# Kernel optimization log

Hardware: AMD Instinct MI355X
Metric: run time of the kernel (lower is better)

The kernel has to match this reference:

```python
import jax, jax.numpy as jnp
import numpy as np

WORD = 512
ED = 64


def setup_inputs() -> dict:
    key = jax.random.key(0)
    ks = jax.random.split(key, 7)
    x = jax.random.normal(ks[0], (4, 4096, WORD), dtype=jnp.float32)
    # Dense layer params (kernel + bias) for query/key/value projections
    s = 1.0 / np.sqrt(WORD)
    Wq = jax.random.normal(ks[1], (WORD, ED), dtype=jnp.float32) * s
    Wk = jax.random.normal(ks[2], (WORD, ED), dtype=jnp.float32) * s
    Wv = jax.random.normal(ks[3], (WORD, ED), dtype=jnp.float32) * s
    bq = jnp.zeros((ED,), dtype=jnp.float32)
    bk = jnp.zeros((ED,), dtype=jnp.float32)
    bv = jnp.zeros((ED,), dtype=jnp.float32)
    return {"x": x, "Wq": Wq, "bq": bq, "Wk": Wk, "bk": bk, "Wv": Wv, "bv": bv}


def reference(x, Wq, bq, Wk, bk, Wv, bv):
    # Q, K, V: [B, S, ED]
    Q = jnp.einsum('bsw,we->bse', x, Wq) + bq
    K = jnp.einsum('bsw,we->bse', x, Wk) + bk
    V = jnp.einsum('bsw,we->bse', x, Wv) + bv
    scale = 1.0 / jnp.sqrt(jnp.float32(ED))
    score = jnp.einsum('bqe,bke->bqk', Q, K) * scale  # [B, S, S]
    attn = jax.nn.softmax(score, axis=-1)
    Z = jnp.einsum('bqk,bke->bqe', attn, V)  # [B, S, ED]
    return Z
```

## Files before the change

### kernel.cpp

```cpp
#include <hip/hip_runtime.h>
#include <cstdint>


typedef __bf16 bf16x8 __attribute__((ext_vector_type(8)));
typedef float f32x4 __attribute__((ext_vector_type(4)));
typedef float f32x16 __attribute__((ext_vector_type(16)));
typedef int i32x2 __attribute__((ext_vector_type(2)));

#define SCALEQ 0.18033688011112042f

#define WT_OFF 0u
#define Q_OFF  262144u
#define KV_OFF 2359296u
#define L_OFF  6553600u
#define OP_OFF 7077888u

#if defined(__has_builtin)
#if __has_builtin(__builtin_amdgcn_permlane32_swap)
#define HAVE_PLSWAP 1
#endif
#if __has_builtin(__builtin_amdgcn_global_load_lds)
#define HAVE_GLL 1
#endif
#endif
#ifndef HAVE_PLSWAP
#define HAVE_PLSWAP 0
#endif
#ifndef HAVE_GLL
#define HAVE_GLL 0
#endif

__device__ __forceinline__ unsigned short bf16_1(float a) {
  unsigned ua = __builtin_bit_cast(unsigned, a);
  ua += 0x7FFFu + ((ua >> 16) & 1u);
  return (unsigned short)(ua >> 16);
}
__device__ __forceinline__ unsigned cvtpk(float lo, float hi) {
  unsigned r;
  asm("v_cvt_pk_bf16_f32 %0, %1, %2" : "=v"(r) : "v"(lo), "v"(hi));
  return r;
}
__device__ __forceinline__ void plswap(unsigned& x, unsigned& y, unsigned hl) {
#if HAVE_PLSWAP
  i32x2 r = __builtin_amdgcn_permlane32_swap((int)x, (int)y, false, false);
  x = (unsigned)r[0];
  y = (unsigned)r[1];
#else
  unsigned xs = (unsigned)__shfl_xor((int)x, 32);
  unsigned ys = (unsigned)__shfl_xor((int)y, 32);
  unsigned nx = hl ? ys : x;
  unsigned ny = hl ? y : xs;
  x = nx;
  y = ny;
#endif
}
#if HAVE_GLL
__device__ __forceinline__ void gll16(const void* g, void* l) {
  __builtin_amdgcn_global_load_lds(
      (const __attribute__((address_space(1))) void*)g,
      (__attribute__((address_space(3))) void*)l, 16, 0, 0);
}
#endif

__global__ __launch_bounds__(256) void prep_w(const float* __restrict__ Wq,
                                              const float* __restrict__ Wk,
                                              const float* __restrict__ Wv,
                                              unsigned short* __restrict__ wt2) {
  unsigned gtid = blockIdx.x * 256u + threadIdx.x;
  unsigned mat = gtid >> 15, rem = gtid & 32767u;
  const float* w = (mat == 0) ? Wq : (mat == 1) ? Wk : Wv;
  float v = w[rem];
  unsigned k = rem >> 6, n = rem & 63u;
  unsigned col = mat * 64u + n;
  unsigned ntg = col >> 4, l15c = col & 15u;
  unsigned kc = k >> 5, quad = (k >> 3) & 3u, j = k & 7u;
  wt2[((ntg * 16u + kc) * 64u + quad * 16u + l15c) * 8u + j] = bf16_1(v);
}

__global__ __launch_bounds__(256, 4) void qkv_proj(
    const float* __restrict__ x, const unsigned short* __restrict__ wt2,
    const float* __restrict__ bq, const float* __restrict__ bk,
    const float* __restrict__ bv, unsigned short* __restrict__ qws,
    unsigned short* __restrict__ kvws) {
  __shared__ __align__(16) char xs[32768];
  __shared__ float biasl[192];
  const unsigned t = threadIdx.x;
  const unsigned row0 = blockIdx.x * 32u;
  const unsigned w = t >> 6, lane = t & 63u, l15 = lane & 15u, quad = lane >> 4;

  if (t < 192u) {
    unsigned mat = t >> 6, n = t & 63u;
    biasl[t] = (mat == 0) ? bq[n] : (mat == 1) ? bk[n] : bv[n];
  }
#pragma unroll
  for (int i = 0; i < 16; i++) {
    unsigned idx4 = t + 256u * (unsigned)i;
    unsigned fidx = idx4 * 4u;
    unsigned row = fidx >> 9, k = fidx & 511u, g = k >> 3;
    float4 f = *(const float4*)(x + row0 * 512u + fidx);
    int2 v = make_int2((int)cvtpk(f.x, f.y), (int)cvtpk(f.z, f.w));
    *(int2*)(xs + row * 1024u + ((g ^ (row & 7u)) << 4) + (k & 7u) * 2u) = v;
  }
  __syncthreads();

  f32x4 acc[2][3];
#pragma unroll
  for (int rg = 0; rg < 2; rg++)
#pragma unroll
    for (int i = 0; i < 3; i++) acc[rg][i] = {0.f, 0.f, 0.f, 0.f};
  const unsigned short* wbase = wt2 + (w * 3u * 1024u + lane) * 8u;

  int4 cur[3], nxt[3];
#pragma unroll
  for (int nt = 0; nt < 3; nt++)
    cur[nt] = *(const int4*)(wbase + (unsigned)nt * 8192u);
  for (unsigned kc = 0; kc < 16u; kc++) {
    if (kc < 15u) {
#pragma unroll
      for (int nt = 0; nt < 3; nt++)
        nxt[nt] = *(const int4*)(wbase + ((unsigned)nt * 16u + kc + 1u) * 512u);
    }
    unsigned ag = kc * 4u + quad;
    unsigned r1 = 16u + l15;
    int4 av0 = *(const int4*)(xs + l15 * 1024u + ((ag ^ (l15 & 7u)) << 4));
    int4 av1 = *(const int4*)(xs + r1 * 1024u + ((ag ^ (r1 & 7u)) << 4));
    bf16x8 a0 = __builtin_bit_cast(bf16x8, av0);
    bf16x8 a1 = __builtin_bit_cast(bf16x8, av1);
#pragma unroll
    for (int nt = 0; nt < 3; nt++)
      acc[0][nt] = __builtin_amdgcn_mfma_f32_16x16x32_bf16(
          a0, __builtin_bit_cast(bf16x8, cur[nt]), acc[0][nt], 0, 0, 0);
#pragma unroll
    for (int nt = 0; nt < 3; nt++)
      acc[1][nt] = __builtin_amdgcn_mfma_f32_16x16x32_bf16(
          a1, __builtin_bit_cast(bf16x8, cur[nt]), acc[1][nt], 0, 0, 0);
#pragma unroll
    for (int nt = 0; nt < 3; nt++) cur[nt] = nxt[nt];
  }
#pragma unroll
  for (int rg = 0; rg < 2; rg++) {
    unsigned sb = row0 + (unsigned)rg * 16u + quad * 4u;
#pragma unroll
    for (int nt = 0; nt < 3; nt++) {
      unsigned col = w * 48u + (unsigned)nt * 16u + l15;
      unsigned mat = col >> 6, n = col & 63u;
      float bb = biasl[col];
      if (mat == 0) {
#pragma unroll
        for (int r = 0; r < 4; r++)
          qws[(sb + (unsigned)r) * 64u + n] =
              bf16_1((acc[rg][nt][r] + bb) * SCALEQ);
      } else if (mat == 1) {
#pragma unroll
        for (int r = 0; r < 4; r++) {
          unsigned s = sb + (unsigned)r;
          unsigned bb2 = s >> 12, tile = (s & 4095u) >> 6, kap = s & 63u;
          kvws[(bb2 * 64u + tile) * 8192u + (n >> 3) * 512u + kap * 8u +
               (n & 7u)] = bf16_1(acc[rg][nt][r] + bb);
        }
      } else {
        unsigned s = sb;
        unsigned bb2 = s >> 12, tile = (s & 4095u) >> 6;
        unsigned kg = (s & 63u) >> 3, j0 = s & 7u;
        int2 pv =
            make_int2((int)cvtpk(acc[rg][nt][0] + bb, acc[rg][nt][1] + bb),
                      (int)cvtpk(acc[rg][nt][2] + bb, acc[rg][nt][3] + bb));
        *(int2*)(kvws + (bb2 * 64u + tile) * 8192u + (8u + kg) * 512u + n * 8u +
                 j0) = pv;
      }
    }
  }
}

__global__ __launch_bounds__(256, 3) void attn(
    const unsigned short* __restrict__ qws,
    const unsigned short* __restrict__ kvws, float* __restrict__ lws,
    unsigned short* __restrict__ opp) {
  __shared__ __align__(16) char sm[34816];
  const unsigned t = threadIdx.x;
  const unsigned w = t >> 6, lane = t & 63u, l31 = lane & 31u, hl = lane >> 5;
  const unsigned bid = blockIdx.x;
  const unsigned ks = bid >> 7;
  const unsigned b = (bid >> 5) & 3u;
  const unsigned qt = bid & 31u;
  const unsigned q0 = qt * 128u + w * 32u;
  const unsigned tile0 = ks * 10u + (ks < 4u ? ks : 4u);
  const unsigned ntl = (ks < 4u) ? 11u : 10u;
  const unsigned short* kvb = kvws + (b * 64u + tile0) * 8192u + lane * 8u;

  bf16x8 qf[4];
#pragma unroll
  for (int kq = 0; kq < 4; kq++)
    qf[kq] = __builtin_bit_cast(
        bf16x8, *(const int4*)(qws + (b * 4096u + q0 + l31) * 64u +
                               (unsigned)kq * 16u + hl * 8u));
  f32x16 accO[2];
#pragma unroll
  for (int dh = 0; dh < 2; dh++)
#pragma unroll
    for (int r = 0; r < 16; r++) accO[dh][r] = 0.f;
  float lsum = 0.f;

#if HAVE_GLL
#define STAGE(kt_, bi_)                                                \
  {                                                                    \
    _Pragma("unroll") for (int i = 0; i < 4; i++) {                    \
      unsigned c = (unsigned)i * 4u + w;                               \
      gll16(kvb + (kt_)*8192u + c * 512u, sm + (bi_)*16384u + c * 1024u); \
    }                                                                  \
  }
  STAGE(0u, 0u);
  __syncthreads();
#else
  int4 stg[4];
#define LOADT(kt_)                                                         \
  {                                                                        \
    _Pragma("unroll") for (int i = 0; i < 4; i++) stg[i] =                 \
        *(const int4*)(kvb + (kt_)*8192u + ((unsigned)i * 4u + w) * 512u); \
  }
  LOADT(0u);
  {
#pragma unroll
    for (int i = 0; i < 4; i++)
      *(int4*)(sm + ((unsigned)i * 4u + w) * 1024u + lane * 16u) = stg[i];
  }
  __syncthreads();
#endif

  for (unsigned kt = 0; kt < ntl; kt++) {
    char* kb = sm + (kt & 1u) * 16384u;
    int4 kfr[8], vfr[8];
#pragma unroll
    for (int kq = 0; kq < 4; kq++)
#pragma unroll
      for (int kh = 0; kh < 2; kh++)
        kfr[kq * 2 + kh] = *(const int4*)(
            kb + (((unsigned)kq * 2u + hl) * 64u + (unsigned)kh * 32u + l31) * 16u);
#pragma unroll
    for (int kqg = 0; kqg < 4; kqg++)
#pragma unroll
      for (int dh = 0; dh < 2; dh++)
        vfr[kqg * 2 + dh] = *(const int4*)(
            kb + 8192u +
            (((unsigned)kqg * 2u + hl) * 64u + (unsigned)dh * 32u + l31) * 16u);
#if HAVE_GLL
    if (kt + 1u < ntl) STAGE(kt + 1u, (kt + 1u) & 1u);
#else
    if (kt + 1u < ntl) LOADT(kt + 1u);
#endif
    __builtin_amdgcn_s_setprio(1);
#pragma unroll
    for (int kh = 0; kh < 2; kh++) {
      f32x16 z;
#pragma unroll
      for (int r = 0; r < 16; r++) z[r] = 0.f;
#pragma unroll
      for (int kq = 0; kq < 4; kq++)
        z = __builtin_amdgcn_mfma_f32_32x32x16_bf16(
            __builtin_bit_cast(bf16x8, kfr[kq * 2 + kh]), qf[kq], z, 0, 0, 0);
#pragma unroll
      for (int r = 0; r < 16; r++) z[r] = __builtin_amdgcn_exp2f(z[r]);
      float s0 = (z[0] + z[1]) + (z[2] + z[3]);
      float s1 = (z[4] + z[5]) + (z[6] + z[7]);
      float s2 = (z[8] + z[9]) + (z[10] + z[11]);
      float s3 = (z[12] + z[13]) + (z[14] + z[15]);
      lsum += (s0 + s1) + (s2 + s3);
      unsigned pk8[8];
#pragma unroll
      for (int c2 = 0; c2 < 4; c2++) {
        pk8[2 * c2] = cvtpk(z[4 * c2 + 0], z[4 * c2 + 1]);
        pk8[2 * c2 + 1] = cvtpk(z[4 * c2 + 2], z[4 * c2 + 3]);
      }
#pragma unroll
      for (int kqpl = 0; kqpl < 2; kqpl++) {
        unsigned a0 = pk8[4 * kqpl + 0], a1 = pk8[4 * kqpl + 1];
        unsigned b0 = pk8[4 * kqpl + 2], b1 = pk8[4 * kqpl + 3];
        plswap(a0, b0, hl);
        plswap(a1, b1, hl);
        int4 fr = make_int4((int)a0, (int)a1, (int)b0, (int)b1);
        bf16x8 pf = __builtin_bit_cast(bf16x8, fr);
        unsigned kqg = (unsigned)kh * 2u + (unsigned)kqpl;
#pragma unroll
        for (int dh = 0; dh < 2; dh++)
          accO[dh] = __builtin_amdgcn_mfma_f32_32x32x16_bf16(
              __builtin_bit_cast(bf16x8, vfr[kqg * 2u + (unsigned)dh]), pf,
              accO[dh], 0, 0, 0);
      }
    }
    __builtin_amdgcn_s_setprio(0);
    __syncthreads();
#if !HAVE_GLL
    if (kt + 1u < ntl) {
#pragma unroll
      for (int i = 0; i < 4; i++)
        *(int4*)(sm + ((kt + 1u) & 1u) * 16384u +
                 ((unsigned)i * 4u + w) * 1024u + lane * 16u) = stg[i];
      __syncthreads();
    }
#endif
  }
  float lt = lsum + __shfl_xor(lsum, 32);
  if (hl == 0u) lws[ks * 16384u + b * 4096u + q0 + l31] = lt;
  float* sc = (float*)(sm + w * 8704u);
#pragma unroll
  for (int dh = 0; dh < 2; dh++)
#pragma unroll
    for (int r = 0; r < 16; r++) {
      unsigned d = (unsigned)dh * 32u + (unsigned)(r & 3) +
                   8u * (unsigned)(r >> 2) + 4u * hl;
      sc[l31 * 68u + d] = accO[dh][r];
    }
#pragma unroll
  for (int i = 0; i < 4; i++) {
    unsigned ql = (lane >> 3) + (unsigned)i * 8u;
    unsigned d0 = (lane & 7u) * 8u;
    float4 f0 = *(const float4*)(sc + ql * 68u + d0);
    float4 f1 = *(const float4*)(sc + ql * 68u + d0 + 4u);
    int4 pv = make_int4((int)cvtpk(f0.x, f0.y), (int)cvtpk(f0.z, f0.w),
                        (int)cvtpk(f1.x, f1.y), (int)cvtpk(f1.z, f1.w));
    *(int4*)(opp + ks * 1048576u + (b * 4096u + q0 + ql) * 64u + d0) = pv;
  }
}

__global__ __launch_bounds__(256) void combine(const unsigned short* __restrict__ opp,
                                               const float* __restrict__ lws,
                                               float* __restrict__ out) {
#pragma unroll
  for (int ii = 0; ii < 2; ii++) {
    unsigned slot = blockIdx.x * 512u + threadIdx.x + 256u * (unsigned)ii;
    unsigned q = slot >> 4, c = (slot & 15u) * 4u;
    float l = 0.f;
#pragma unroll
    for (int s = 0; s < 6; s++) l += lws[(unsigned)s * 16384u + q];
    float inv = 1.0f / l;
    float4 r = make_float4(0.f, 0.f, 0.f, 0.f);
#pragma unroll
    for (int s = 0; s < 6; s++) {
      int2 pv = *(const int2*)(opp + (unsigned)s * 1048576u + q * 64u + c);
      r.x += __builtin_bit_cast(float, (unsigned)pv.x << 16);
      r.y += __builtin_bit_cast(float, (unsigned)pv.x & 0xFFFF0000u);
      r.z += __builtin_bit_cast(float, (unsigned)pv.y << 16);
      r.w += __builtin_bit_cast(float, (unsigned)pv.y & 0xFFFF0000u);
    }
    r.x *= inv; r.y *= inv; r.z *= inv; r.w *= inv;
    *(float4*)(out + q * 64u + c) = r;
  }
}

extern "C" void kernel_launch(void* const* d_in, const int* in_sizes, int n_in,
                              void* d_out, int out_size, void* d_ws,
                              size_t ws_size, hipStream_t stream) {
  const float* x = (const float*)d_in[0];
  const float* Wq = (const float*)d_in[1];
  const float* bq = (const float*)d_in[2];
  const float* Wk = (const float*)d_in[3];
  const float* bk = (const float*)d_in[4];
  const float* Wv = (const float*)d_in[5];
  const float* bv = (const float*)d_in[6];
  char* ws = (char*)d_ws;
  unsigned short* wt2 = (unsigned short*)(ws + WT_OFF);
  unsigned short* qb = (unsigned short*)(ws + Q_OFF);
  unsigned short* kvb = (unsigned short*)(ws + KV_OFF);
  float* lp = (float*)(ws + L_OFF);
  unsigned short* opp = (unsigned short*)(ws + OP_OFF);
  float* outp = (float*)d_out;

  prep_w<<<384, 256, 0, stream>>>(Wq, Wk, Wv, wt2);
  qkv_proj<<<512, 256, 0, stream>>>(x, wt2, bq, bk, bv, qb, kvb);
  attn<<<768, 256, 0, stream>>>(qb, kvb, lp, opp);
  combine<<<512, 256, 0, stream>>>(opp, lp, outp);
}
```

Baseline: 117.1 us.

## Give each attention warp two query tiles and switch to eight KV splits

Each warp now processes 64 query rows (two 32-row tiles) against every K/V tile it loads from LDS, so the K and V fragments are reused twice per LDS read. The KV split is regularised to 8 splits of 8 tiles each, with 512 blocks instead of 768, and the combine kernel is updated to sum 8 partials. This is meant to halve LDS K/V traffic per query and increase MFMA density per loaded fragment. In exchange it raises register pressure (launch bound drops to 2 blocks per CU), writes more partial outputs, and makes the combine step read more data.

```diff
diff --git a/kernel.cpp b/kernel.cpp
--- a/kernel.cpp
+++ b/kernel.cpp
@@ -172,7 +172,7 @@
   }
 }
 
-__global__ __launch_bounds__(256, 3) void attn(
+__global__ __launch_bounds__(256, 2) void attn(
     const unsigned short* __restrict__ qws,
     const unsigned short* __restrict__ kvws, float* __restrict__ lws,
     unsigned short* __restrict__ opp) {
@@ -180,26 +180,29 @@
   const unsigned t = threadIdx.x;
   const unsigned w = t >> 6, lane = t & 63u, l31 = lane & 31u, hl = lane >> 5;
   const unsigned bid = blockIdx.x;
-  const unsigned ks = bid >> 7;
-  const unsigned b = (bid >> 5) & 3u;
-  const unsigned qt = bid & 31u;
-  const unsigned q0 = qt * 128u + w * 32u;
-  const unsigned tile0 = ks * 10u + (ks < 4u ? ks : 4u);
-  const unsigned ntl = (ks < 4u) ? 11u : 10u;
-  const unsigned short* kvb = kvws + (b * 64u + tile0) * 8192u + lane * 8u;
-
-  bf16x8 qf[4];
-#pragma unroll
-  for (int kq = 0; kq < 4; kq++)
-    qf[kq] = __builtin_bit_cast(
-        bf16x8, *(const int4*)(qws + (b * 4096u + q0 + l31) * 64u +
-                               (unsigned)kq * 16u + hl * 8u));
-  f32x16 accO[2];
-#pragma unroll
-  for (int dh = 0; dh < 2; dh++)
-#pragma unroll
-    for (int r = 0; r < 16; r++) accO[dh][r] = 0.f;
-  float lsum = 0.f;
+  const unsigned ks = bid >> 6;
+  const unsigned qb = bid & 63u;
+  const unsigned b = qb >> 4;
+  const unsigned s0 = (qb & 15u) * 256u + w * 64u;
+  const unsigned short* kvb = kvws + (b * 64u + ks * 8u) * 8192u + lane * 8u;
+
+  bf16x8 qf[2][4];
+#pragma unroll
+  for (int qt2 = 0; qt2 < 2; qt2++)
+#pragma unroll
+    for (int kq = 0; kq < 4; kq++)
+      qf[qt2][kq] = __builtin_bit_cast(
+          bf16x8,
+          *(const int4*)(qws + (b * 4096u + s0 + (unsigned)qt2 * 32u + l31) * 64u +
+                         (unsigned)kq * 16u + hl * 8u));
+  f32x16 accO[2][2];
+#pragma unroll
+  for (int qt2 = 0; qt2 < 2; qt2++)
+#pragma unroll
+    for (int dh = 0; dh < 2; dh++)
+#pragma unroll
+      for (int r = 0; r < 16; r++) accO[qt2][dh][r] = 0.f;
+  float lsumA = 0.f, lsumB = 0.f;
 
 #if HAVE_GLL
 #define STAGE(kt_, bi_)                                                \
@@ -227,7 +230,8 @@
   __syncthreads();
 #endif
 
-  for (unsigned kt = 0; kt < ntl; kt++) {
+#pragma unroll 1
+  for (unsigned kt = 0; kt < 8u; kt++) {
     char* kb = sm + (kt & 1u) * 16384u;
     int4 kfr[8], vfr[8];
 #pragma unroll
@@ -244,53 +248,81 @@
             kb + 8192u +
             (((unsigned)kqg * 2u + hl) * 64u + (unsigned)dh * 32u + l31) * 16u);
 #if HAVE_GLL
-    if (kt + 1u < ntl) STAGE(kt + 1u, (kt + 1u) & 1u);
+    if (kt < 7u) STAGE(kt + 1u, (kt + 1u) & 1u);
 #else
-    if (kt + 1u < ntl) LOADT(kt + 1u);
+    if (kt < 7u) LOADT(kt + 1u);
 #endif
     __builtin_amdgcn_s_setprio(1);
 #pragma unroll
     for (int kh = 0; kh < 2; kh++) {
-      f32x16 z;
-#pragma unroll
-      for (int r = 0; r < 16; r++) z[r] = 0.f;
+      f32x16 zA, zB;
+#pragma unroll
+      for (int r = 0; r < 16; r++) zA[r] = 0.f;
+#pragma unroll
+      for (int r = 0; r < 16; r++) zB[r] = 0.f;
 #pragma unroll
       for (int kq = 0; kq < 4; kq++)
-        z = __builtin_amdgcn_mfma_f32_32x32x16_bf16(
-            __builtin_bit_cast(bf16x8, kfr[kq * 2 + kh]), qf[kq], z, 0, 0, 0);
-#pragma unroll
-      for (int r = 0; r < 16; r++) z[r] = __builtin_amdgcn_exp2f(z[r]);
-      float s0 = (z[0] + z[1]) + (z[2] + z[3]);
-      float s1 = (z[4] + z[5]) + (z[6] + z[7]);
-      float s2 = (z[8] + z[9]) + (z[10] + z[11]);
-      float s3 = (z[12] + z[13]) + (z[14] + z[15]);
-      lsum += (s0 + s1) + (s2 + s3);
-      unsigned pk8[8];
+        zA = __builtin_amdgcn_mfma_f32_32x32x16_bf16(
+            __builtin_bit_cast(bf16x8, kfr[kq * 2 + kh]), qf[0][kq], zA, 0, 0, 0);
+#pragma unroll
+      for (int kq = 0; kq < 4; kq++)
+        zB = __builtin_amdgcn_mfma_f32_32x32x16_bf16(
+            __builtin_bit_cast(bf16x8, kfr[kq * 2 + kh]), qf[1][kq], zB, 0, 0, 0);
+#pragma unroll
+      for (int r = 0; r < 16; r++) zA[r] = __builtin_amdgcn_exp2f(zA[r]);
+#pragma unroll
+      for (int r = 0; r < 16; r++) zB[r] = __builtin_amdgcn_exp2f(zB[r]);
+      {
+        float s0a = (zA[0] + zA[1]) + (zA[2] + zA[3]);
+        float s1a = (zA[4] + zA[5]) + (zA[6] + zA[7]);
+        float s2a = (zA[8] + zA[9]) + (zA[10] + zA[11]);
+        float s3a = (zA[12] + zA[13]) + (zA[14] + zA[15]);
+        lsumA += (s0a + s1a) + (s2a + s3a);
+        float s0b = (zB[0] + zB[1]) + (zB[2] + zB[3]);
+        float s1b = (zB[4] + zB[5]) + (zB[6] + zB[7]);
+        float s2b = (zB[8] + zB[9]) + (zB[10] + zB[11]);
+        float s3b = (zB[12] + zB[13]) + (zB[14] + zB[15]);
+        lsumB += (s0b + s1b) + (s2b + s3b);
+      }
+      unsigned pkA[8], pkB[8];
 #pragma unroll
       for (int c2 = 0; c2 < 4; c2++) {
-        pk8[2 * c2] = cvtpk(z[4 * c2 + 0], z[4 * c2 + 1]);
-        pk8[2 * c2 + 1] = cvtpk(z[4 * c2 + 2], z[4 * c2 + 3]);
+        pkA[2 * c2] = cvtpk(zA[4 * c2 + 0], zA[4 * c2 + 1]);
+        pkA[2 * c2 + 1] = cvtpk(zA[4 * c2 + 2], zA[4 * c2 + 3]);
+        pkB[2 * c2] = cvtpk(zB[4 * c2 + 0], zB[4 * c2 + 1]);
+        pkB[2 * c2 + 1] = cvtpk(zB[4 * c2 + 2], zB[4 * c2 + 3]);
       }
 #pragma unroll
       for (int kqpl = 0; kqpl < 2; kqpl++) {
-        unsigned a0 = pk8[4 * kqpl + 0], a1 = pk8[4 * kqpl + 1];
-        unsigned b0 = pk8[4 * kqpl + 2], b1 = pk8[4 * kqpl + 3];
+        unsigned kqg = (unsigned)kh * 2u + (unsigned)kqpl;
+        unsigned a0 = pkA[4 * kqpl + 0], a1 = pkA[4 * kqpl + 1];
+        unsigned b0 = pkA[4 * kqpl + 2], b1 = pkA[4 * kqpl + 3];
         plswap(a0, b0, hl);
         plswap(a1, b1, hl);
-        int4 fr = make_int4((int)a0, (int)a1, (int)b0, (int)b1);
-        bf16x8 pf = __builtin_bit_cast(bf16x8, fr);
-        unsigned kqg = (unsigned)kh * 2u + (unsigned)kqpl;
+        int4 frA = make_int4((int)a0, (int)a1, (int)b0, (int)b1);
+        bf16x8 pfA = __builtin_bit_cast(bf16x8, frA);
 #pragma unroll
         for (int dh = 0; dh < 2; dh++)
-          accO[dh] = __builtin_amdgcn_mfma_f32_32x32x16_bf16(
-              __builtin_bit_cast(bf16x8, vfr[kqg * 2u + (unsigned)dh]), pf,
-              accO[dh], 0, 0, 0);
+          accO[0][dh] = __builtin_amdgcn_mfma_f32_32x32x16_bf16(
+              __builtin_bit_cast(bf16x8, vfr[kqg * 2u + (unsigned)dh]), pfA,
+              accO[0][dh], 0, 0, 0);
+        unsigned c0 = pkB[4 * kqpl + 0], c1 = pkB[4 * kqpl + 1];
+        unsigned d0 = pkB[4 * kqpl + 2], d1 = pkB[4 * kqpl + 3];
+        plswap(c0, d0, hl);
+        plswap(c1, d1, hl);
+        int4 frB = make_int4((int)c0, (int)c1, (int)d0, (int)d1);
+        bf16x8 pfB = __builtin_bit_cast(bf16x8, frB);
+#pragma unroll
+        for (int dh = 0; dh < 2; dh++)
+          accO[1][dh] = __builtin_amdgcn_mfma_f32_32x32x16_bf16(
+              __builtin_bit_cast(bf16x8, vfr[kqg * 2u + (unsigned)dh]), pfB,
+              accO[1][dh], 0, 0, 0);
       }
     }
     __builtin_amdgcn_s_setprio(0);
     __syncthreads();
 #if !HAVE_GLL
-    if (kt + 1u < ntl) {
+    if (kt < 7u) {
 #pragma unroll
       for (int i = 0; i < 4; i++)
         *(int4*)(sm + ((kt + 1u) & 1u) * 16384u +
@@ -299,26 +331,31 @@
     }
 #endif
   }
-  float lt = lsum + __shfl_xor(lsum, 32);
-  if (hl == 0u) lws[ks * 16384u + b * 4096u + q0 + l31] = lt;
   float* sc = (float*)(sm + w * 8704u);
 #pragma unroll
-  for (int dh = 0; dh < 2; dh++)
-#pragma unroll
-    for (int r = 0; r < 16; r++) {
-      unsigned d = (unsigned)dh * 32u + (unsigned)(r & 3) +
-                   8u * (unsigned)(r >> 2) + 4u * hl;
-      sc[l31 * 68u + d] = accO[dh][r];
-    }
-#pragma unroll
-  for (int i = 0; i < 4; i++) {
-    unsigned ql = (lane >> 3) + (unsigned)i * 8u;
-    unsigned d0 = (lane & 7u) * 8u;
-    float4 f0 = *(const float4*)(sc + ql * 68u + d0);
-    float4 f1 = *(const float4*)(sc + ql * 68u + d0 + 4u);
-    int4 pv = make_int4((int)cvtpk(f0.x, f0.y), (int)cvtpk(f0.z, f0.w),
-                        (int)cvtpk(f1.x, f1.y), (int)cvtpk(f1.z, f1.w));
-    *(int4*)(opp + ks * 1048576u + (b * 4096u + q0 + ql) * 64u + d0) = pv;
+  for (int qt2 = 0; qt2 < 2; qt2++) {
+    float ls = (qt2 == 0) ? lsumA : lsumB;
+    float lt = ls + __shfl_xor(ls, 32);
+    unsigned qrow = s0 + (unsigned)qt2 * 32u;
+    if (hl == 0u) lws[ks * 16384u + b * 4096u + qrow + l31] = lt;
+#pragma unroll
+    for (int dh = 0; dh < 2; dh++)
+#pragma unroll
+      for (int r = 0; r < 16; r++) {
+        unsigned d = (unsigned)dh * 32u + (unsigned)(r & 3) +
+                     8u * (unsigned)(r >> 2) + 4u * hl;
+        sc[l31 * 68u + d] = accO[qt2][dh][r];
+      }
+#pragma unroll
+    for (int i = 0; i < 4; i++) {
+      unsigned ql = (lane >> 3) + (unsigned)i * 8u;
+      unsigned d0 = (lane & 7u) * 8u;
+      float4 f0 = *(const float4*)(sc + ql * 68u + d0);
+      float4 f1 = *(const float4*)(sc + ql * 68u + d0 + 4u);
+      int4 pv = make_int4((int)cvtpk(f0.x, f0.y), (int)cvtpk(f0.z, f0.w),
+                          (int)cvtpk(f1.x, f1.y), (int)cvtpk(f1.z, f1.w));
+      *(int4*)(opp + ks * 1048576u + (b * 4096u + qrow + ql) * 64u + d0) = pv;
+    }
   }
 }
 
@@ -331,11 +368,11 @@
     unsigned q = slot >> 4, c = (slot & 15u) * 4u;
     float l = 0.f;
 #pragma unroll
-    for (int s = 0; s < 6; s++) l += lws[(unsigned)s * 16384u + q];
+    for (int s = 0; s < 8; s++) l += lws[(unsigned)s * 16384u + q];
     float inv = 1.0f / l;
     float4 r = make_float4(0.f, 0.f, 0.f, 0.f);
 #pragma unroll
-    for (int s = 0; s < 6; s++) {
+    for (int s = 0; s < 8; s++) {
       int2 pv = *(const int2*)(opp + (unsigned)s * 1048576u + q * 64u + c);
       r.x += __builtin_bit_cast(float, (unsigned)pv.x << 16);
       r.y += __builtin_bit_cast(float, (unsigned)pv.x & 0xFFFF0000u);
@@ -367,6 +404,6 @@
 
   prep_w<<<384, 256, 0, stream>>>(Wq, Wk, Wv, wt2);
   qkv_proj<<<512, 256, 0, stream>>>(x, wt2, bq, bk, bv, qb, kvb);
-  attn<<<768, 256, 0, stream>>>(qb, kvb, lp, opp);
+  attn<<<512, 256, 0, stream>>>(qb, kvb, lp, opp);
   combine<<<512, 256, 0, stream>>>(opp, lp, outp);
 }
```

Result: no change. 115.7 us, median of 2 (-1.2%).
